# Performance work log

Hardware: AMD Instinct MI355X
Metric: run time of the kernel (lower is better)

Reference implementation:

```python
import jax, jax.numpy as jnp
import numpy as np

N_NODES = 50000
N_EDGES = 800000
IN_CH = 128
HEADS = 4
OUT_CH = 32
NEG_SLOPE = 0.2


def setup_inputs() -> dict:
    key = jax.random.key(0)
    ks = jax.random.split(key, 8)
    x = jax.random.normal(ks[0], (N_NODES, IN_CH), dtype=jnp.float32)
    # edges guaranteed to have no self-loops (module removes then re-adds them)
    tgt = jax.random.randint(ks[1], (N_EDGES,), 0, N_NODES)
    off = jax.random.randint(ks[2], (N_EDGES,), 1, N_NODES)
    src = (tgt + off) % N_NODES
    edge_index = jnp.stack([src, tgt]).astype(jnp.int64)
    glorot = lambda k, shp: jax.random.uniform(
        k, shp, jnp.float32, -1.0, 1.0) * np.sqrt(6.0 / (shp[-1] + shp[-2]))
    Wl = glorot(ks[3], (HEADS * OUT_CH, IN_CH))  # torch Linear weight [out,in]
    Wr = glorot(ks[4], (HEADS * OUT_CH, IN_CH))
    att = glorot(ks[5], (1, HEADS, OUT_CH))
    bl = jnp.zeros((HEADS * OUT_CH,), jnp.float32)
    br = jnp.zeros((HEADS * OUT_CH,), jnp.float32)
    bias = jnp.zeros((HEADS * OUT_CH,), jnp.float32)
    return {"x": x, "edge_index": edge_index, "Wl": Wl, "bl": bl,
            "Wr": Wr, "br": br, "att": att, "bias": bias}


def _forward(x, edge_index, Wl, bl, Wr, br, att, bias):
    H, C = HEADS, OUT_CH
    n = x.shape[0]
    x_l = (x @ Wl.T + bl).reshape(n, H, C)  # target projection
    x_r = (x @ Wr.T + br).reshape(n, H, C)  # source projection
    # add self-loops (inputs contain none by construction)
    loops = jnp.arange(n, dtype=edge_index.dtype)
    src = jnp.concatenate([edge_index[0], loops])
    tgt = jnp.concatenate([edge_index[1], loops])
    x_i = x_l[tgt]                     # [E', H, C]
    x_j = x_r[src]                     # [E', H, C]
    a_in = jax.nn.leaky_relu(x_i + x_j, NEG_SLOPE)
    alpha = jnp.einsum('ehc,ohc->eh', a_in, att)  # [E', H]
    # segment softmax over target nodes
    m = jax.ops.segment_max(alpha, tgt, num_segments=n)
    alpha = jnp.exp(alpha - jax.lax.stop_gradient(m)[tgt])
    denom = jax.ops.segment_sum(alpha, tgt, num_segments=n)
    alpha = alpha / denom[tgt]
    msgs = x_j * alpha[:, :, None]     # [E', H, C]
    out = jax.ops.segment_sum(msgs, tgt, num_segments=n)  # [N, H, C]
    out = out.reshape(n, H * C) + bias  # concat=True
    return out


def reference(x, edge_index, Wl, bl, Wr, br, att, bias):
    return _forward(x, edge_index, Wl, bl, Wr, br, att, bias)
```

## Files before the change

### kernel.cpp

```cpp
#include <hip/hip_runtime.h>
#include <hip/hip_bf16.h>
#include <stdint.h>

#define N_NODES 50000
#define N_EDGES 800000
#define IN_CH   128
#define NEG_SLOPE 0.2f

#define PROJ_BLOCKS 782
#define E_PER 8
#define FILL_BLOCKS 391

typedef short short8 __attribute__((ext_vector_type(8)));
typedef float f32x4  __attribute__((ext_vector_type(4)));
typedef float f32x2  __attribute__((ext_vector_type(2)));

static __device__ __forceinline__ float bf_lo(uint32_t p) { return __uint_as_float(p << 16); }
static __device__ __forceinline__ float bf_hi(uint32_t p) { return __uint_as_float(p & 0xffff0000u); }
static __device__ __forceinline__ uint16_t f_to_bf(float f) {
    uint32_t u = __float_as_uint(f);
    u += 0x7fffu + ((u >> 16) & 1u);
    return (uint16_t)(u >> 16);
}
static __device__ __forceinline__ float lrelu(float x) { return fmaxf(x, NEG_SLOPE * x); }

static __device__ __forceinline__ float sum16(float x) {
    x += __uint_as_float(__builtin_amdgcn_update_dpp(0, __float_as_uint(x), 0xB1,  0xf, 0xf, true));
    x += __uint_as_float(__builtin_amdgcn_update_dpp(0, __float_as_uint(x), 0x4E,  0xf, 0xf, true));
    x += __uint_as_float(__builtin_amdgcn_update_dpp(0, __float_as_uint(x), 0x141, 0xf, 0xf, true));
    x += __uint_as_float(__builtin_amdgcn_update_dpp(0, __float_as_uint(x), 0x140, 0xf, 0xf, true));
    return x;
}

__global__ __launch_bounds__(256) void prep_kernel(
    const float* __restrict__ Wl, const float* __restrict__ Wr,
    __hip_bfloat16* __restrict__ wswz, int* __restrict__ cnt)
{
    int t = blockIdx.x * 256 + threadIdx.x;
    if (t < 4096) {
        int ct = t >> 8, rem = t & 255;
        int ch = rem >> 6, lane = rem & 63;
        int m = lane & 15, quad = lane >> 4;
        const float* W = (ct < 8) ? Wl : Wr;
        int o = ((ct & 7) << 4) + m;
        const float* src = W + (size_t)o * IN_CH + ch * 32 + quad * 8;
        short8 f;
#pragma unroll
        for (int j = 0; j < 8; ++j) f[j] = (short)f_to_bf(src[j]);
        *(short8*)((short*)wswz + (size_t)t * 8) = f;
    }
    for (int i = t; i < N_NODES; i += 64 * 256) cnt[i] = 0;
}

__global__ __launch_bounds__(256) void mid_kernel(
    const float* __restrict__ x,
    const __hip_bfloat16* __restrict__ wswz,
    const float* __restrict__ bl, const float* __restrict__ br,
    float* __restrict__ xl, __hip_bfloat16* __restrict__ xr,
    const int* __restrict__ ei, int cap,
    int* __restrict__ cnt, uint16_t* __restrict__ csr)
{
    if (blockIdx.x < PROJ_BLOCKS) {
        int wave = blockIdx.x * 4 + (threadIdx.x >> 6);
        int rowbase = wave * 16;
        if (rowbase >= N_NODES) return;
        int lane = threadIdx.x & 63;
        int m = lane & 15;
        int quad = lane >> 4;

        short8 afrag[4];
        const float* xrow = x + (size_t)(rowbase + m) * IN_CH;
#pragma unroll
        for (int ch = 0; ch < 4; ++ch) {
            f32x4 p0 = *(const f32x4*)(xrow + ch * 32 + quad * 8);
            f32x4 p1 = *(const f32x4*)(xrow + ch * 32 + quad * 8 + 4);
            short8 f;
#pragma unroll
            for (int j = 0; j < 4; ++j) { f[j] = (short)f_to_bf(p0[j]); f[j + 4] = (short)f_to_bf(p1[j]); }
            afrag[ch] = f;
        }

        const short* wz = (const short*)wswz;
#pragma unroll
        for (int ct = 0; ct < 16; ++ct) {
            const float* bv = (ct < 8) ? bl : br;
            int o = ((ct & 7) << 4) + m;
            f32x4 acc = {0.f, 0.f, 0.f, 0.f};
#pragma unroll
            for (int ch = 0; ch < 4; ++ch) {
                short8 bfrag = *(const short8*)(wz + ((size_t)(ct * 4 + ch) * 64 + lane) * 8);
                acc = __builtin_amdgcn_mfma_f32_16x16x32_bf16(afrag[ch], bfrag, acc, 0, 0, 0);
            }
            float bias_v = bv[o];
            if (ct < 8) {
#pragma unroll
                for (int r = 0; r < 4; ++r)
                    xl[(size_t)(rowbase + quad * 4 + r) * IN_CH + o] = acc[r] + bias_v;
            } else {
#pragma unroll
                for (int r = 0; r < 4; ++r)
                    xr[(size_t)(rowbase + quad * 4 + r) * IN_CH + o] = __float2bfloat16(acc[r] + bias_v);
            }
        }
    } else {
        const uint32_t* eiw = (const uint32_t*)ei;
        bool z = (eiw[2 * (threadIdx.x & 63) + 1] == 0u);
        bool is64 = __popcll(__ballot(z)) >= 32;

        int tid = (blockIdx.x - PROJ_BLOCKS) * 256 + threadIdx.x;
        int e0 = tid * E_PER;
        if (e0 >= N_EDGES) return;

        int src[E_PER], tgt[E_PER];
        if (is64) {
            const int4* ps = (const int4*)(eiw + 2 * (size_t)e0);
            const int4* pt = (const int4*)(eiw + 2 * ((size_t)N_EDGES + e0));
#pragma unroll
            for (int k = 0; k < 4; ++k) {
                int4 s = ps[k], t = pt[k];
                src[2 * k] = s.x; src[2 * k + 1] = s.z;
                tgt[2 * k] = t.x; tgt[2 * k + 1] = t.z;
            }
        } else {
            const int4* ps = (const int4*)(ei + e0);
            const int4* pt = (const int4*)(ei + N_EDGES + e0);
#pragma unroll
            for (int k = 0; k < 2; ++k) {
                int4 s = ps[k], t = pt[k];
                src[4 * k] = s.x; src[4 * k + 1] = s.y; src[4 * k + 2] = s.z; src[4 * k + 3] = s.w;
                tgt[4 * k] = t.x; tgt[4 * k + 1] = t.y; tgt[4 * k + 2] = t.z; tgt[4 * k + 3] = t.w;
            }
        }

        int pos[E_PER];
#pragma unroll
        for (int k = 0; k < E_PER; ++k) {
            bool ok = (unsigned)src[k] < N_NODES && (unsigned)tgt[k] < N_NODES;
            pos[k] = ok ? atomicAdd(&cnt[tgt[k]], 1) : cap;
        }
#pragma unroll
        for (int k = 0; k < E_PER; ++k)
            if (pos[k] < cap)
                __builtin_nontemporal_store((uint16_t)src[k],
                                            &csr[(size_t)tgt[k] * cap + pos[k]]);
    }
}

__global__ __launch_bounds__(256) void agg_kernel(
    const __hip_bfloat16* __restrict__ xr,
    const int* __restrict__ cnt, const uint16_t* __restrict__ csr, int cap,
    const float* __restrict__ att, const float* __restrict__ bias,
    float* out )
{
    int n = blockIdx.x * 4 + (threadIdx.x >> 6);
    if (n >= N_NODES) return;
    int lane = threadIdx.x & 63;

    const uint32_t* xrw = (const uint32_t*)xr;

    f32x2 qv = *(const f32x2*)(out + (size_t)n * IN_CH + 2 * lane);
    f32x2 av = *(const f32x2*)(att + 2 * lane);
    f32x2 bv = *(const f32x2*)(bias + 2 * lane);

    int deg = min(cnt[n], cap);
    const uint16_t* lst = csr + (size_t)n * cap;
    int idxreg = (int)lst[min(lane, cap - 1)];

    uint32_t u = xrw[(size_t)n * 64 + lane];
    float v0 = bf_lo(u), v1 = bf_hi(u);
    float t = sum16(lrelu(qv[0] + v0) * av[0] + lrelu(qv[1] + v1) * av[1]);
    float w = __expf(t);
    float lsum = w;
    float acc0 = w * v0, acc1 = w * v1;

    if (deg > 0) {
        int dm1 = deg - 1;
        int s0a = __builtin_amdgcn_readlane(idxreg, 0);
        int s0b = __builtin_amdgcn_readlane(idxreg, min(1, dm1));
        int s1a = __builtin_amdgcn_readlane(idxreg, min(2, dm1));
        int s1b = __builtin_amdgcn_readlane(idxreg, min(3, dm1));
        uint32_t uA0 = xrw[(size_t)s0a * 64 + lane];
        uint32_t uB0 = xrw[(size_t)s0b * 64 + lane];
        uint32_t uA1 = xrw[(size_t)s1a * 64 + lane];
        uint32_t uB1 = xrw[(size_t)s1b * 64 + lane];
        int i = 0;
        while (i + 1 < deg) {
            int s2a = __builtin_amdgcn_readlane(idxreg, min(i + 4, dm1));
            int s2b = __builtin_amdgcn_readlane(idxreg, min(i + 5, dm1));
            uint32_t uA2 = xrw[(size_t)s2a * 64 + lane];
            uint32_t uB2 = xrw[(size_t)s2b * 64 + lane];

            float a0 = bf_lo(uA0), a1 = bf_hi(uA0);
            float b0 = bf_lo(uB0), b1 = bf_hi(uB0);
            float tA = sum16(lrelu(qv[0] + a0) * av[0] + lrelu(qv[1] + a1) * av[1]);
            float tB = sum16(lrelu(qv[0] + b0) * av[0] + lrelu(qv[1] + b1) * av[1]);
            float wA = __expf(tA), wB = __expf(tB);
            lsum += wA + wB;
            acc0 += wA * a0 + wB * b0;
            acc1 += wA * a1 + wB * b1;

            uA0 = uA1; uB0 = uB1;
            uA1 = uA2; uB1 = uB2;
            i += 2;
        }
        if (i < deg) {
            float a0 = bf_lo(uA0), a1 = bf_hi(uA0);
            float tA = sum16(lrelu(qv[0] + a0) * av[0] + lrelu(qv[1] + a1) * av[1]);
            float wA = __expf(tA);
            lsum += wA;
            acc0 += wA * a0;
            acc1 += wA * a1;
        }
    }

    float inv = 1.f / lsum;
    f32x2 ov;
    ov[0] = acc0 * inv + bv[0];
    ov[1] = acc1 * inv + bv[1];
    *(f32x2*)(out + (size_t)n * IN_CH + 2 * lane) = ov;
}

extern "C" void kernel_launch(void* const* d_in, const int* in_sizes, int n_in,
                              void* d_out, int out_size, void* d_ws, size_t ws_size,
                              hipStream_t stream) {
    const float* x    = (const float*)d_in[0];
    const int*   ei   = (const int*)d_in[1];
    const float* Wl   = (const float*)d_in[2];
    const float* bl   = (const float*)d_in[3];
    const float* Wr   = (const float*)d_in[4];
    const float* br   = (const float*)d_in[5];
    const float* att  = (const float*)d_in[6];
    const float* bias = (const float*)d_in[7];
    float* out = (float*)d_out;

    const size_t CSR_BASE = 13065536;
    char* ws = (char*)d_ws;
    __hip_bfloat16* xr   = (__hip_bfloat16*)(ws);
    __hip_bfloat16* wswz = (__hip_bfloat16*)(ws + 12800000);
    int*      cnt = (int*)(ws + 12865536);
    uint16_t* csr = (uint16_t*)(ws + CSR_BASE);

    long long avail = (ws_size > CSR_BASE) ? (long long)(ws_size - CSR_BASE) : 0;
    int cap = (int)(avail / ((long long)N_NODES * 2));
    if (cap > 64) cap = 64;
    if (cap < 1)  cap = 1;

    prep_kernel<<<64, 256, 0, stream>>>(Wl, Wr, wswz, cnt);
    mid_kernel<<<PROJ_BLOCKS + FILL_BLOCKS, 256, 0, stream>>>(
        x, wswz, bl, br, out, xr, ei, cap, cnt, csr);
    agg_kernel<<<N_NODES / 4, 256, 0, stream>>>(xr, cnt, csr, cap, att, bias, out);
}
```

Measured before the change: 195.6 us.

## Interleave per-node counter and neighbor list into one 128-byte slab

Packs each node's atomic degree counter and its bucketed source-index list into a single 128-byte slab, so the count and list share a cache line for both the atomic fill and the aggregation read. The list capacity drops from 64 to 62, and prep now zeroes the whole 6.4MB slab region instead of 200KB of counters. The nontemporal store is replaced by a normal store, which may keep lines cached near the atomics. The extra zeroing traffic and the lower capacity, which truncates nodes with more than 62 neighbours, are the trade-offs.

```diff
diff --git a/kernel.cpp b/kernel.cpp
--- a/kernel.cpp
+++ b/kernel.cpp
@@ -14,6 +14,7 @@
 typedef short short8 __attribute__((ext_vector_type(8)));
 typedef float f32x4  __attribute__((ext_vector_type(4)));
 typedef float f32x2  __attribute__((ext_vector_type(2)));
+typedef int   i32x4  __attribute__((ext_vector_type(4)));
 
 static __device__ __forceinline__ float bf_lo(uint32_t p) { return __uint_as_float(p << 16); }
 static __device__ __forceinline__ float bf_hi(uint32_t p) { return __uint_as_float(p & 0xffff0000u); }
@@ -34,7 +35,7 @@
 
 __global__ __launch_bounds__(256) void prep_kernel(
     const float* __restrict__ Wl, const float* __restrict__ Wr,
-    __hip_bfloat16* __restrict__ wswz, int* __restrict__ cnt)
+    __hip_bfloat16* __restrict__ wswz, i32x4* __restrict__ zbase, int zchunks)
 {
     int t = blockIdx.x * 256 + threadIdx.x;
     if (t < 4096) {
@@ -49,7 +50,8 @@
         for (int j = 0; j < 8; ++j) f[j] = (short)f_to_bf(src[j]);
         *(short8*)((short*)wswz + (size_t)t * 8) = f;
     }
-    for (int i = t; i < N_NODES; i += 64 * 256) cnt[i] = 0;
+    i32x4 z = {0, 0, 0, 0};
+    for (int i = t; i < zchunks; i += 64 * 256) zbase[i] = z;
 }
 
 __global__ __launch_bounds__(256) void mid_kernel(
@@ -58,7 +60,8 @@
     const float* __restrict__ bl, const float* __restrict__ br,
     float* __restrict__ xl, __hip_bfloat16* __restrict__ xr,
     const int* __restrict__ ei, int cap,
-    int* __restrict__ cnt, uint16_t* __restrict__ csr)
+    char* __restrict__ cbase, int cstride,
+    char* __restrict__ ebase, int estride)
 {
     if (blockIdx.x < PROJ_BLOCKS) {
         int wave = blockIdx.x * 4 + (threadIdx.x >> 6);
@@ -136,19 +139,20 @@
 #pragma unroll
         for (int k = 0; k < E_PER; ++k) {
             bool ok = (unsigned)src[k] < N_NODES && (unsigned)tgt[k] < N_NODES;
-            pos[k] = ok ? atomicAdd(&cnt[tgt[k]], 1) : cap;
+            pos[k] = ok ? atomicAdd((int*)(cbase + (size_t)tgt[k] * cstride), 1)
+                        : cap;
         }
 #pragma unroll
         for (int k = 0; k < E_PER; ++k)
             if (pos[k] < cap)
-                __builtin_nontemporal_store((uint16_t)src[k],
-                                            &csr[(size_t)tgt[k] * cap + pos[k]]);
+                *(uint16_t*)(ebase + (size_t)tgt[k] * estride + 2 * pos[k]) = (uint16_t)src[k];
     }
 }
 
 __global__ __launch_bounds__(256) void agg_kernel(
     const __hip_bfloat16* __restrict__ xr,
-    const int* __restrict__ cnt, const uint16_t* __restrict__ csr, int cap,
+    const char* __restrict__ cbase, int cstride,
+    const char* __restrict__ ebase, int estride, int cap,
     const float* __restrict__ att, const float* __restrict__ bias,
     float* out )
 {
@@ -162,8 +166,8 @@
     f32x2 av = *(const f32x2*)(att + 2 * lane);
     f32x2 bv = *(const f32x2*)(bias + 2 * lane);
 
-    int deg = min(cnt[n], cap);
-    const uint16_t* lst = csr + (size_t)n * cap;
+    int deg = min(*(const int*)(cbase + (size_t)n * cstride), cap);
+    const uint16_t* lst = (const uint16_t*)(ebase + (size_t)n * estride);
     int idxreg = (int)lst[min(lane, cap - 1)];
 
     uint32_t u = xrw[(size_t)n * 64 + lane];
@@ -233,20 +237,34 @@
     const float* bias = (const float*)d_in[7];
     float* out = (float*)d_out;
 
-    const size_t CSR_BASE = 13065536;
     char* ws = (char*)d_ws;
     __hip_bfloat16* xr   = (__hip_bfloat16*)(ws);
     __hip_bfloat16* wswz = (__hip_bfloat16*)(ws + 12800000);
-    int*      cnt = (int*)(ws + 12865536);
-    uint16_t* csr = (uint16_t*)(ws + CSR_BASE);
-
-    long long avail = (ws_size > CSR_BASE) ? (long long)(ws_size - CSR_BASE) : 0;
-    int cap = (int)(avail / ((long long)N_NODES * 2));
-    if (cap > 64) cap = 64;
-    if (cap < 1)  cap = 1;
-
-    prep_kernel<<<64, 256, 0, stream>>>(Wl, Wr, wswz, cnt);
+
+    const size_t SLAB_BASE = 12865536;
+    char* cbase; char* ebase;
+    int cstride, estride, cap;
+    size_t zbytes;
+    if (ws_size >= SLAB_BASE + (size_t)N_NODES * 128) {
+        cbase = ws + SLAB_BASE;  cstride = 128;
+        ebase = cbase + 4;       estride = 128;
+        cap = 62;
+        zbytes = (size_t)N_NODES * 128;
+    } else {
+        cbase = ws + SLAB_BASE;  cstride = 4;
+        ebase = ws + SLAB_BASE + 200000;
+        long long avail = (ws_size > SLAB_BASE + 200000)
+                        ? (long long)(ws_size - SLAB_BASE - 200000) : 0;
+        cap = (int)(avail / ((long long)N_NODES * 2));
+        if (cap > 64) cap = 64;
+        if (cap < 1)  cap = 1;
+        estride = 2 * cap;
+        zbytes = 200000;
+    }
+
+    prep_kernel<<<64, 256, 0, stream>>>(Wl, Wr, wswz, (i32x4*)cbase, (int)(zbytes / 16));
     mid_kernel<<<PROJ_BLOCKS + FILL_BLOCKS, 256, 0, stream>>>(
-        x, wswz, bl, br, out, xr, ei, cap, cnt, csr);
-    agg_kernel<<<N_NODES / 4, 256, 0, stream>>>(xr, cnt, csr, cap, att, bias, out);
-}
+        x, wswz, bl, br, out, xr, ei, cap, cbase, cstride, ebase, estride);
+    agg_kernel<<<N_NODES / 4, 256, 0, stream>>>(
+        xr, cbase, cstride, ebase, estride, cap, att, bias, out);
+}
```

New measurement: 180.9 us. -7.5%, faster.

## Build CSR via per-block LDS histograms, scan and scatter instead of global atomics

Applied to the files above, without the earlier changes.

Replaces the global-atomic counting fill with a three-pass counting sort. Each of B blocks builds a packed 8-bit per-node histogram of its edge slice in shared memory, a scan kernel turns the per-block histograms into offsets and packed degrees, and a scatter kernel writes source ids into a fixed 64-wide CSR using shared-memory atomics. The projection now runs as its own kernel. The aim is to avoid contended global atomics and their scattered writes. The cost is extra launches, low block counts in the histogram and scatter passes, loss of overlap between projection and fill, and degrees assumed to fit in 8 bits. The old path is kept as a fallback when the workspace is too small.

```diff
diff --git a/kernel.cpp b/kernel.cpp
--- a/kernel.cpp
+++ b/kernel.cpp
@@ -10,10 +10,12 @@
 #define PROJ_BLOCKS 782
 #define E_PER 8
 #define FILL_BLOCKS 391
+#define HIST_WORDS 12500
 
 typedef short short8 __attribute__((ext_vector_type(8)));
 typedef float f32x4  __attribute__((ext_vector_type(4)));
 typedef float f32x2  __attribute__((ext_vector_type(2)));
+typedef int   i32x4  __attribute__((ext_vector_type(4)));
 
 static __device__ __forceinline__ float bf_lo(uint32_t p) { return __uint_as_float(p << 16); }
 static __device__ __forceinline__ float bf_hi(uint32_t p) { return __uint_as_float(p & 0xffff0000u); }
@@ -32,76 +34,200 @@
     return x;
 }
 
-__global__ __launch_bounds__(256) void prep_kernel(
+static __device__ __forceinline__ void proj_body(
+    int wave, int lane,
+    const float* __restrict__ x, const __hip_bfloat16* __restrict__ wswz,
+    const float* __restrict__ bl, const float* __restrict__ br,
+    float* __restrict__ xl, __hip_bfloat16* __restrict__ xr)
+{
+    int rowbase = wave * 16;
+    if (rowbase >= N_NODES) return;
+    int m = lane & 15;
+    int quad = lane >> 4;
+
+    short8 afrag[4];
+    const float* xrow = x + (size_t)(rowbase + m) * IN_CH;
+#pragma unroll
+    for (int ch = 0; ch < 4; ++ch) {
+        f32x4 p0 = *(const f32x4*)(xrow + ch * 32 + quad * 8);
+        f32x4 p1 = *(const f32x4*)(xrow + ch * 32 + quad * 8 + 4);
+        short8 f;
+#pragma unroll
+        for (int j = 0; j < 4; ++j) { f[j] = (short)f_to_bf(p0[j]); f[j + 4] = (short)f_to_bf(p1[j]); }
+        afrag[ch] = f;
+    }
+
+    const short* wz = (const short*)wswz;
+#pragma unroll
+    for (int ct = 0; ct < 16; ++ct) {
+        const float* bv = (ct < 8) ? bl : br;
+        int o = ((ct & 7) << 4) + m;
+        f32x4 acc = {0.f, 0.f, 0.f, 0.f};
+#pragma unroll
+        for (int ch = 0; ch < 4; ++ch) {
+            short8 bfrag = *(const short8*)(wz + ((size_t)(ct * 4 + ch) * 64 + lane) * 8);
+            acc = __builtin_amdgcn_mfma_f32_16x16x32_bf16(afrag[ch], bfrag, acc, 0, 0, 0);
+        }
+        float bias_v = bv[o];
+        if (ct < 8) {
+#pragma unroll
+            for (int r = 0; r < 4; ++r)
+                xl[(size_t)(rowbase + quad * 4 + r) * IN_CH + o] = acc[r] + bias_v;
+        } else {
+#pragma unroll
+            for (int r = 0; r < 4; ++r)
+                xr[(size_t)(rowbase + quad * 4 + r) * IN_CH + o] = __float2bfloat16(acc[r] + bias_v);
+        }
+    }
+}
+
+static __device__ __forceinline__ void wswz_body(
+    int t, const float* __restrict__ Wl, const float* __restrict__ Wr,
+    __hip_bfloat16* __restrict__ wswz)
+{
+    int ct = t >> 8, rem = t & 255;
+    int ch = rem >> 6, lane = rem & 63;
+    int m = lane & 15, quad = lane >> 4;
+    const float* W = (ct < 8) ? Wl : Wr;
+    int o = ((ct & 7) << 4) + m;
+    const float* src = W + (size_t)o * IN_CH + ch * 32 + quad * 8;
+    short8 f;
+#pragma unroll
+    for (int j = 0; j < 8; ++j) f[j] = (short)f_to_bf(src[j]);
+    *(short8*)((short*)wswz + (size_t)t * 8) = f;
+}
+
+
+__global__ __launch_bounds__(256) void prep_sort(
+    const float* __restrict__ Wl, const float* __restrict__ Wr,
+    __hip_bfloat16* __restrict__ wswz,
+    const int* __restrict__ ei, uint32_t* __restrict__ H, int EPB)
+{
+    __shared__ uint32_t hist[HIST_WORDS];
+    int tid = threadIdx.x;
+    if (blockIdx.x < 16) {
+        wswz_body(blockIdx.x * 256 + tid, Wl, Wr, wswz);
+        return;
+    }
+    int fb = blockIdx.x - 16;
+    for (int w = tid; w < HIST_WORDS; w += 256) hist[w] = 0;
+    __syncthreads();
+
+    const uint32_t* eiw = (const uint32_t*)ei;
+    bool z = (eiw[2 * (tid & 63) + 1] == 0u);
+    bool is64 = __popcll(__ballot(z)) >= 32;
+    int e0 = fb * EPB;
+    if (is64) {
+        const uint2* e64 = (const uint2*)eiw;
+        for (int k = tid; k < EPB; k += 256) {
+            int e = e0 + k;
+            int s = (int)e64[e].x;
+            int t = (int)e64[(size_t)N_EDGES + e].x;
+            if ((unsigned)s < N_NODES && (unsigned)t < N_NODES)
+                atomicAdd(&hist[t >> 2], 1u << ((t & 3) * 8));
+        }
+    } else {
+        for (int k = tid; k < EPB; k += 256) {
+            int e = e0 + k;
+            int s = ei[e], t = ei[N_EDGES + e];
+            if ((unsigned)s < N_NODES && (unsigned)t < N_NODES)
+                atomicAdd(&hist[t >> 2], 1u << ((t & 3) * 8));
+        }
+    }
+    __syncthreads();
+    uint32_t* Hb = H + (size_t)fb * HIST_WORDS;
+    for (int w = tid; w < HIST_WORDS; w += 256) Hb[w] = hist[w];
+}
+
+__global__ __launch_bounds__(256) void proj_kernel(
+    const float* __restrict__ x, const __hip_bfloat16* __restrict__ wswz,
+    const float* __restrict__ bl, const float* __restrict__ br,
+    float* __restrict__ xl, __hip_bfloat16* __restrict__ xr)
+{
+    proj_body(blockIdx.x * 4 + (threadIdx.x >> 6), threadIdx.x & 63,
+              x, wswz, bl, br, xl, xr);
+}
+
+__global__ __launch_bounds__(256) void scan_kernel(
+    uint32_t* __restrict__ H, int B, uint32_t* __restrict__ degs)
+{
+    int w = blockIdx.x * 256 + threadIdx.x;
+    if (w >= HIST_WORDS) return;
+    uint32_t acc = 0;
+    for (int c = 0; c < B; c += 16) {
+        uint32_t v[16];
+#pragma unroll
+        for (int j = 0; j < 16; ++j) v[j] = H[(size_t)(c + j) * HIST_WORDS + w];
+#pragma unroll
+        for (int j = 0; j < 16; ++j) {
+            uint32_t t = v[j];
+            H[(size_t)(c + j) * HIST_WORDS + w] = acc;
+            acc += t;
+        }
+    }
+    degs[w] = acc;
+}
+
+__global__ __launch_bounds__(256) void scatter_kernel(
+    const int* __restrict__ ei, const uint32_t* __restrict__ H, int EPB,
+    uint16_t* __restrict__ csr)
+{
+    __shared__ uint32_t hist[HIST_WORDS];
+    int fb = blockIdx.x, tid = threadIdx.x;
+    const uint32_t* Hb = H + (size_t)fb * HIST_WORDS;
+    for (int w = tid; w < HIST_WORDS; w += 256) hist[w] = Hb[w];
+    __syncthreads();
+
+    const uint32_t* eiw = (const uint32_t*)ei;
+    bool z = (eiw[2 * (tid & 63) + 1] == 0u);
+    bool is64 = __popcll(__ballot(z)) >= 32;
+    int e0 = fb * EPB;
+    if (is64) {
+        const uint2* e64 = (const uint2*)eiw;
+        for (int k = tid; k < EPB; k += 256) {
+            int e = e0 + k;
+            int s = (int)e64[e].x;
+            int t = (int)e64[(size_t)N_EDGES + e].x;
+            if ((unsigned)s < N_NODES && (unsigned)t < N_NODES) {
+                uint32_t sh = (t & 3) * 8;
+                uint32_t old = atomicAdd(&hist[t >> 2], 1u << sh);
+                uint32_t pos = (old >> sh) & 255u;
+                if (pos < 64u) csr[(size_t)t * 64 + pos] = (uint16_t)s;
+            }
+        }
+    } else {
+        for (int k = tid; k < EPB; k += 256) {
+            int e = e0 + k;
+            int s = ei[e], t = ei[N_EDGES + e];
+            if ((unsigned)s < N_NODES && (unsigned)t < N_NODES) {
+                uint32_t sh = (t & 3) * 8;
+                uint32_t old = atomicAdd(&hist[t >> 2], 1u << sh);
+                uint32_t pos = (old >> sh) & 255u;
+                if (pos < 64u) csr[(size_t)t * 64 + pos] = (uint16_t)s;
+            }
+        }
+    }
+}
+
+__global__ __launch_bounds__(256) void prep_legacy(
     const float* __restrict__ Wl, const float* __restrict__ Wr,
     __hip_bfloat16* __restrict__ wswz, int* __restrict__ cnt)
 {
     int t = blockIdx.x * 256 + threadIdx.x;
-    if (t < 4096) {
-        int ct = t >> 8, rem = t & 255;
-        int ch = rem >> 6, lane = rem & 63;
-        int m = lane & 15, quad = lane >> 4;
-        const float* W = (ct < 8) ? Wl : Wr;
-        int o = ((ct & 7) << 4) + m;
-        const float* src = W + (size_t)o * IN_CH + ch * 32 + quad * 8;
-        short8 f;
-#pragma unroll
-        for (int j = 0; j < 8; ++j) f[j] = (short)f_to_bf(src[j]);
-        *(short8*)((short*)wswz + (size_t)t * 8) = f;
-    }
+    if (t < 4096) wswz_body(t, Wl, Wr, wswz);
     for (int i = t; i < N_NODES; i += 64 * 256) cnt[i] = 0;
 }
 
-__global__ __launch_bounds__(256) void mid_kernel(
-    const float* __restrict__ x,
-    const __hip_bfloat16* __restrict__ wswz,
+__global__ __launch_bounds__(256) void mid_legacy(
+    const float* __restrict__ x, const __hip_bfloat16* __restrict__ wswz,
     const float* __restrict__ bl, const float* __restrict__ br,
     float* __restrict__ xl, __hip_bfloat16* __restrict__ xr,
     const int* __restrict__ ei, int cap,
     int* __restrict__ cnt, uint16_t* __restrict__ csr)
 {
     if (blockIdx.x < PROJ_BLOCKS) {
-        int wave = blockIdx.x * 4 + (threadIdx.x >> 6);
-        int rowbase = wave * 16;
-        if (rowbase >= N_NODES) return;
-        int lane = threadIdx.x & 63;
-        int m = lane & 15;
-        int quad = lane >> 4;
-
-        short8 afrag[4];
-        const float* xrow = x + (size_t)(rowbase + m) * IN_CH;
-#pragma unroll
-        for (int ch = 0; ch < 4; ++ch) {
-            f32x4 p0 = *(const f32x4*)(xrow + ch * 32 + quad * 8);
-            f32x4 p1 = *(const f32x4*)(xrow + ch * 32 + quad * 8 + 4);
-            short8 f;
-#pragma unroll
-            for (int j = 0; j < 4; ++j) { f[j] = (short)f_to_bf(p0[j]); f[j + 4] = (short)f_to_bf(p1[j]); }
-            afrag[ch] = f;
-        }
-
-        const short* wz = (const short*)wswz;
-#pragma unroll
-        for (int ct = 0; ct < 16; ++ct) {
-            const float* bv = (ct < 8) ? bl : br;
-            int o = ((ct & 7) << 4) + m;
-            f32x4 acc = {0.f, 0.f, 0.f, 0.f};
-#pragma unroll
-            for (int ch = 0; ch < 4; ++ch) {
-                short8 bfrag = *(const short8*)(wz + ((size_t)(ct * 4 + ch) * 64 + lane) * 8);
-                acc = __builtin_amdgcn_mfma_f32_16x16x32_bf16(afrag[ch], bfrag, acc, 0, 0, 0);
-            }
-            float bias_v = bv[o];
-            if (ct < 8) {
-#pragma unroll
-                for (int r = 0; r < 4; ++r)
-                    xl[(size_t)(rowbase + quad * 4 + r) * IN_CH + o] = acc[r] + bias_v;
-            } else {
-#pragma unroll
-                for (int r = 0; r < 4; ++r)
-                    xr[(size_t)(rowbase + quad * 4 + r) * IN_CH + o] = __float2bfloat16(acc[r] + bias_v);
-            }
-        }
+        proj_body(blockIdx.x * 4 + (threadIdx.x >> 6), threadIdx.x & 63,
+                  x, wswz, bl, br, xl, xr);
     } else {
         const uint32_t* eiw = (const uint32_t*)ei;
         bool z = (eiw[2 * (threadIdx.x & 63) + 1] == 0u);
@@ -140,15 +266,14 @@
         }
 #pragma unroll
         for (int k = 0; k < E_PER; ++k)
-            if (pos[k] < cap)
-                __builtin_nontemporal_store((uint16_t)src[k],
-                                            &csr[(size_t)tgt[k] * cap + pos[k]]);
+            if (pos[k] < cap) csr[(size_t)tgt[k] * cap + pos[k]] = (uint16_t)src[k];
     }
 }
 
 __global__ __launch_bounds__(256) void agg_kernel(
     const __hip_bfloat16* __restrict__ xr,
-    const int* __restrict__ cnt, const uint16_t* __restrict__ csr, int cap,
+    const char* __restrict__ degbase, int degpacked,
+    const uint16_t* __restrict__ csr, int ldcsr, int cap,
     const float* __restrict__ att, const float* __restrict__ bias,
     float* out )
 {
@@ -162,8 +287,16 @@
     f32x2 av = *(const f32x2*)(att + 2 * lane);
     f32x2 bv = *(const f32x2*)(bias + 2 * lane);
 
-    int deg = min(cnt[n], cap);
-    const uint16_t* lst = csr + (size_t)n * cap;
+    int deg;
+    if (degpacked) {
+        uint32_t pk = ((const uint32_t*)degbase)[n >> 2];
+        deg = (int)((pk >> ((n & 3) * 8)) & 255u);
+    } else {
+        deg = *(const int*)(degbase + (size_t)n * 4);
+    }
+    deg = min(deg, cap);
+
+    const uint16_t* lst = csr + (size_t)n * ldcsr;
     int idxreg = (int)lst[min(lane, cap - 1)];
 
     uint32_t u = xrw[(size_t)n * 64 + lane];
@@ -233,20 +366,44 @@
     const float* bias = (const float*)d_in[7];
     float* out = (float*)d_out;
 
-    const size_t CSR_BASE = 13065536;
     char* ws = (char*)d_ws;
     __hip_bfloat16* xr   = (__hip_bfloat16*)(ws);
     __hip_bfloat16* wswz = (__hip_bfloat16*)(ws + 12800000);
-    int*      cnt = (int*)(ws + 12865536);
-    uint16_t* csr = (uint16_t*)(ws + CSR_BASE);
-
-    long long avail = (ws_size > CSR_BASE) ? (long long)(ws_size - CSR_BASE) : 0;
-    int cap = (int)(avail / ((long long)N_NODES * 2));
-    if (cap > 64) cap = 64;
-    if (cap < 1)  cap = 1;
-
-    prep_kernel<<<64, 256, 0, stream>>>(Wl, Wr, wswz, cnt);
-    mid_kernel<<<PROJ_BLOCKS + FILL_BLOCKS, 256, 0, stream>>>(
-        x, wswz, bl, br, out, xr, ei, cap, cnt, csr);
-    agg_kernel<<<N_NODES / 4, 256, 0, stream>>>(xr, cnt, csr, cap, att, bias, out);
-}
+    const size_t AFTER = 12865536;
+
+    int B = 0;
+    {
+        size_t need64 = AFTER + (size_t)64 * 50000 + 50048 + 6400000;
+        size_t need16 = AFTER + (size_t)16 * 50000 + 50048 + 6400000;
+        if (ws_size >= need64) B = 64;
+        else if (ws_size >= need16) B = 16;
+    }
+
+    if (B) {
+        uint32_t* H    = (uint32_t*)(ws + AFTER);
+        uint32_t* degs = (uint32_t*)(ws + AFTER + (size_t)B * 50000);
+        uint16_t* csr  = (uint16_t*)(ws + AFTER + (size_t)B * 50000 + 50048);
+        int EPB = N_EDGES / B;
+
+        prep_sort<<<16 + B, 256, 0, stream>>>(Wl, Wr, wswz, ei, H, EPB);
+        proj_kernel<<<PROJ_BLOCKS, 256, 0, stream>>>(x, wswz, bl, br, out, xr);
+        scan_kernel<<<49, 256, 0, stream>>>(H, B, degs);
+        scatter_kernel<<<B, 256, 0, stream>>>(ei, H, EPB, csr);
+        agg_kernel<<<N_NODES / 4, 256, 0, stream>>>(
+            xr, (const char*)degs, 1, csr, 64, 64, att, bias, out);
+    } else {
+        int* cnt      = (int*)(ws + AFTER);
+        uint16_t* csr = (uint16_t*)(ws + AFTER + 200000);
+        long long avail = (ws_size > AFTER + 200000)
+                        ? (long long)(ws_size - AFTER - 200000) : 0;
+        int cap = (int)(avail / ((long long)N_NODES * 2));
+        if (cap > 64) cap = 64;
+        if (cap < 1)  cap = 1;
+
+        prep_legacy<<<64, 256, 0, stream>>>(Wl, Wr, wswz, cnt);
+        mid_legacy<<<PROJ_BLOCKS + FILL_BLOCKS, 256, 0, stream>>>(
+            x, wswz, bl, br, out, xr, ei, cap, cnt, csr);
+        agg_kernel<<<N_NODES / 4, 256, 0, stream>>>(
+            xr, (const char*)cnt, 0, csr, cap, cap, att, bias, out);
+    }
+}
```

Measured after the change: 203.3 us. 3.9% more time.

## Split fused projection/CSR kernel and vectorize aggregation with packed math and paired DPP reductions

Applied to the files above, without the earlier changes.

Splits the merged projection-plus-CSR-fill kernel into separate fill and projection launches. The projection now gives each block 16 rows with the four waves sharing the column tiles, rather than each wave computing all 16 tiles. The aggregation loop switches to f32x2 packed arithmetic and an inline-asm DPP reduction that interleaves two edge scores, aiming to hide DPP latency. The CSR store loses its nontemporal hint, the split adds a launch and removes the overlap between fill and projection, and each wave now redoes the x-fragment load and bf16 conversion.

```diff
diff --git a/kernel.cpp b/kernel.cpp
--- a/kernel.cpp
+++ b/kernel.cpp
@@ -7,7 +7,6 @@
 #define IN_CH   128
 #define NEG_SLOPE 0.2f
 
-#define PROJ_BLOCKS 782
 #define E_PER 8
 #define FILL_BLOCKS 391
 
@@ -22,7 +21,14 @@
     u += 0x7fffu + ((u >> 16) & 1u);
     return (uint16_t)(u >> 16);
 }
-static __device__ __forceinline__ float lrelu(float x) { return fmaxf(x, NEG_SLOPE * x); }
+
+static __device__ __forceinline__ f32x2 lrelu2(f32x2 x) {
+    f32x2 s = x * NEG_SLOPE;
+    f32x2 r;
+    r[0] = fmaxf(x[0], s[0]);
+    r[1] = fmaxf(x[1], s[1]);
+    return r;
+}
 
 static __device__ __forceinline__ float sum16(float x) {
     x += __uint_as_float(__builtin_amdgcn_update_dpp(0, __float_as_uint(x), 0xB1,  0xf, 0xf, true));
@@ -30,6 +36,19 @@
     x += __uint_as_float(__builtin_amdgcn_update_dpp(0, __float_as_uint(x), 0x141, 0xf, 0xf, true));
     x += __uint_as_float(__builtin_amdgcn_update_dpp(0, __float_as_uint(x), 0x140, 0xf, 0xf, true));
     return x;
+}
+
+static __device__ __forceinline__ void sum16x2(float& a, float& b) {
+    asm("s_nop 0\n\t"
+        "v_add_f32 %0, %0, %0 quad_perm:[1,0,3,2] row_mask:0xf bank_mask:0xf bound_ctrl:0\n\t"
+        "v_add_f32 %1, %1, %1 quad_perm:[1,0,3,2] row_mask:0xf bank_mask:0xf bound_ctrl:0\n\t"
+        "v_add_f32 %0, %0, %0 quad_perm:[2,3,0,1] row_mask:0xf bank_mask:0xf bound_ctrl:0\n\t"
+        "v_add_f32 %1, %1, %1 quad_perm:[2,3,0,1] row_mask:0xf bank_mask:0xf bound_ctrl:0\n\t"
+        "v_add_f32 %0, %0, %0 row_half_mirror row_mask:0xf bank_mask:0xf bound_ctrl:0\n\t"
+        "v_add_f32 %1, %1, %1 row_half_mirror row_mask:0xf bank_mask:0xf bound_ctrl:0\n\t"
+        "v_add_f32 %0, %0, %0 row_mirror row_mask:0xf bank_mask:0xf bound_ctrl:0\n\t"
+        "v_add_f32 %1, %1, %1 row_mirror row_mask:0xf bank_mask:0xf bound_ctrl:0"
+        : "+v"(a), "+v"(b));
 }
 
 __global__ __launch_bounds__(256) void prep_kernel(
@@ -52,97 +71,95 @@
     for (int i = t; i < N_NODES; i += 64 * 256) cnt[i] = 0;
 }
 
-__global__ __launch_bounds__(256) void mid_kernel(
-    const float* __restrict__ x,
-    const __hip_bfloat16* __restrict__ wswz,
-    const float* __restrict__ bl, const float* __restrict__ br,
-    float* __restrict__ xl, __hip_bfloat16* __restrict__ xr,
+__global__ __launch_bounds__(256) void fill_kernel(
     const int* __restrict__ ei, int cap,
     int* __restrict__ cnt, uint16_t* __restrict__ csr)
 {
-    if (blockIdx.x < PROJ_BLOCKS) {
-        int wave = blockIdx.x * 4 + (threadIdx.x >> 6);
-        int rowbase = wave * 16;
-        if (rowbase >= N_NODES) return;
-        int lane = threadIdx.x & 63;
-        int m = lane & 15;
-        int quad = lane >> 4;
-
-        short8 afrag[4];
-        const float* xrow = x + (size_t)(rowbase + m) * IN_CH;
+    const uint32_t* eiw = (const uint32_t*)ei;
+    bool z = (eiw[2 * (threadIdx.x & 63) + 1] == 0u);
+    bool is64 = __popcll(__ballot(z)) >= 32;
+
+    int tid = blockIdx.x * 256 + threadIdx.x;
+    int e0 = tid * E_PER;
+    if (e0 >= N_EDGES) return;
+
+    int src[E_PER], tgt[E_PER];
+    if (is64) {
+        const int4* ps = (const int4*)(eiw + 2 * (size_t)e0);
+        const int4* pt = (const int4*)(eiw + 2 * ((size_t)N_EDGES + e0));
+#pragma unroll
+        for (int k = 0; k < 4; ++k) {
+            int4 s = ps[k], t = pt[k];
+            src[2 * k] = s.x; src[2 * k + 1] = s.z;
+            tgt[2 * k] = t.x; tgt[2 * k + 1] = t.z;
+        }
+    } else {
+        const int4* ps = (const int4*)(ei + e0);
+        const int4* pt = (const int4*)(ei + N_EDGES + e0);
+#pragma unroll
+        for (int k = 0; k < 2; ++k) {
+            int4 s = ps[k], t = pt[k];
+            src[4 * k] = s.x; src[4 * k + 1] = s.y; src[4 * k + 2] = s.z; src[4 * k + 3] = s.w;
+            tgt[4 * k] = t.x; tgt[4 * k + 1] = t.y; tgt[4 * k + 2] = t.z; tgt[4 * k + 3] = t.w;
+        }
+    }
+
+    int pos[E_PER];
+#pragma unroll
+    for (int k = 0; k < E_PER; ++k) {
+        bool ok = (unsigned)src[k] < N_NODES && (unsigned)tgt[k] < N_NODES;
+        pos[k] = ok ? atomicAdd(&cnt[tgt[k]], 1) : cap;
+    }
+#pragma unroll
+    for (int k = 0; k < E_PER; ++k)
+        if (pos[k] < cap) csr[(size_t)tgt[k] * cap + pos[k]] = (uint16_t)src[k];
+}
+
+__global__ __launch_bounds__(256) void proj_kernel(
+    const float* __restrict__ x, const __hip_bfloat16* __restrict__ wswz,
+    const float* __restrict__ bl, const float* __restrict__ br,
+    float* __restrict__ xl, __hip_bfloat16* __restrict__ xr)
+{
+    int rowbase = blockIdx.x * 16;
+    int lane = threadIdx.x & 63;
+    int widx = threadIdx.x >> 6;
+    int m = lane & 15;
+    int quad = lane >> 4;
+
+    short8 afrag[4];
+    const float* xrow = x + (size_t)(rowbase + m) * IN_CH;
+#pragma unroll
+    for (int ch = 0; ch < 4; ++ch) {
+        f32x4 p0 = *(const f32x4*)(xrow + ch * 32 + quad * 8);
+        f32x4 p1 = *(const f32x4*)(xrow + ch * 32 + quad * 8 + 4);
+        short8 f;
+#pragma unroll
+        for (int j = 0; j < 4; ++j) { f[j] = (short)f_to_bf(p0[j]); f[j + 4] = (short)f_to_bf(p1[j]); }
+        afrag[ch] = f;
+    }
+
+    const short* wz = (const short*)wswz;
+    const float* bv = (widx < 2) ? bl : br;
+#pragma unroll
+    for (int cc = 0; cc < 4; ++cc) {
+        int ct = widx * 4 + cc;
+        int o = ((ct & 7) << 4) + m;
+        f32x4 acc = {0.f, 0.f, 0.f, 0.f};
 #pragma unroll
         for (int ch = 0; ch < 4; ++ch) {
-            f32x4 p0 = *(const f32x4*)(xrow + ch * 32 + quad * 8);
-            f32x4 p1 = *(const f32x4*)(xrow + ch * 32 + quad * 8 + 4);
-            short8 f;
-#pragma unroll
-            for (int j = 0; j < 4; ++j) { f[j] = (short)f_to_bf(p0[j]); f[j + 4] = (short)f_to_bf(p1[j]); }
-            afrag[ch] = f;
-        }
-
-        const short* wz = (const short*)wswz;
-#pragma unroll
-        for (int ct = 0; ct < 16; ++ct) {
-            const float* bv = (ct < 8) ? bl : br;
-            int o = ((ct & 7) << 4) + m;
-            f32x4 acc = {0.f, 0.f, 0.f, 0.f};
-#pragma unroll
-            for (int ch = 0; ch < 4; ++ch) {
-                short8 bfrag = *(const short8*)(wz + ((size_t)(ct * 4 + ch) * 64 + lane) * 8);
-                acc = __builtin_amdgcn_mfma_f32_16x16x32_bf16(afrag[ch], bfrag, acc, 0, 0, 0);
-            }
-            float bias_v = bv[o];
-            if (ct < 8) {
-#pragma unroll
-                for (int r = 0; r < 4; ++r)
-                    xl[(size_t)(rowbase + quad * 4 + r) * IN_CH + o] = acc[r] + bias_v;
-            } else {
-#pragma unroll
-                for (int r = 0; r < 4; ++r)
-                    xr[(size_t)(rowbase + quad * 4 + r) * IN_CH + o] = __float2bfloat16(acc[r] + bias_v);
-            }
-        }
-    } else {
-        const uint32_t* eiw = (const uint32_t*)ei;
-        bool z = (eiw[2 * (threadIdx.x & 63) + 1] == 0u);
-        bool is64 = __popcll(__ballot(z)) >= 32;
-
-        int tid = (blockIdx.x - PROJ_BLOCKS) * 256 + threadIdx.x;
-        int e0 = tid * E_PER;
-        if (e0 >= N_EDGES) return;
-
-        int src[E_PER], tgt[E_PER];
-        if (is64) {
-            const int4* ps = (const int4*)(eiw + 2 * (size_t)e0);
-            const int4* pt = (const int4*)(eiw + 2 * ((size_t)N_EDGES + e0));
-#pragma unroll
-            for (int k = 0; k < 4; ++k) {
-                int4 s = ps[k], t = pt[k];
-                src[2 * k] = s.x; src[2 * k + 1] = s.z;
-                tgt[2 * k] = t.x; tgt[2 * k + 1] = t.z;
-            }
+            short8 bfrag = *(const short8*)(wz + ((size_t)(ct * 4 + ch) * 64 + lane) * 8);
+            acc = __builtin_amdgcn_mfma_f32_16x16x32_bf16(afrag[ch], bfrag, acc, 0, 0, 0);
+        }
+        float bias_v = bv[o];
+        if (widx < 2) {
+#pragma unroll
+            for (int r = 0; r < 4; ++r)
+                xl[(size_t)(rowbase + quad * 4 + r) * IN_CH + o] = acc[r] + bias_v;
         } else {
-            const int4* ps = (const int4*)(ei + e0);
-            const int4* pt = (const int4*)(ei + N_EDGES + e0);
-#pragma unroll
-            for (int k = 0; k < 2; ++k) {
-                int4 s = ps[k], t = pt[k];
-                src[4 * k] = s.x; src[4 * k + 1] = s.y; src[4 * k + 2] = s.z; src[4 * k + 3] = s.w;
-                tgt[4 * k] = t.x; tgt[4 * k + 1] = t.y; tgt[4 * k + 2] = t.z; tgt[4 * k + 3] = t.w;
-            }
-        }
-
-        int pos[E_PER];
-#pragma unroll
-        for (int k = 0; k < E_PER; ++k) {
-            bool ok = (unsigned)src[k] < N_NODES && (unsigned)tgt[k] < N_NODES;
-            pos[k] = ok ? atomicAdd(&cnt[tgt[k]], 1) : cap;
-        }
-#pragma unroll
-        for (int k = 0; k < E_PER; ++k)
-            if (pos[k] < cap)
-                __builtin_nontemporal_store((uint16_t)src[k],
-                                            &csr[(size_t)tgt[k] * cap + pos[k]]);
+#pragma unroll
+            for (int r = 0; r < 4; ++r)
+                xr[(size_t)(rowbase + quad * 4 + r) * IN_CH + o] = __float2bfloat16(acc[r] + bias_v);
+        }
     }
 }
 
@@ -167,11 +184,12 @@
     int idxreg = (int)lst[min(lane, cap - 1)];
 
     uint32_t u = xrw[(size_t)n * 64 + lane];
-    float v0 = bf_lo(u), v1 = bf_hi(u);
-    float t = sum16(lrelu(qv[0] + v0) * av[0] + lrelu(qv[1] + v1) * av[1]);
+    f32x2 a0v; a0v[0] = bf_lo(u); a0v[1] = bf_hi(u);
+    f32x2 p0 = lrelu2(qv + a0v) * av;
+    float t = sum16(p0[0] + p0[1]);
     float w = __expf(t);
     float lsum = w;
-    float acc0 = w * v0, acc1 = w * v1;
+    f32x2 acc = w * a0v;
 
     if (deg > 0) {
         int dm1 = deg - 1;
@@ -190,33 +208,34 @@
             uint32_t uA2 = xrw[(size_t)s2a * 64 + lane];
             uint32_t uB2 = xrw[(size_t)s2b * 64 + lane];
 
-            float a0 = bf_lo(uA0), a1 = bf_hi(uA0);
-            float b0 = bf_lo(uB0), b1 = bf_hi(uB0);
-            float tA = sum16(lrelu(qv[0] + a0) * av[0] + lrelu(qv[1] + a1) * av[1]);
-            float tB = sum16(lrelu(qv[0] + b0) * av[0] + lrelu(qv[1] + b1) * av[1]);
+            f32x2 aA; aA[0] = bf_lo(uA0); aA[1] = bf_hi(uA0);
+            f32x2 aB; aB[0] = bf_lo(uB0); aB[1] = bf_hi(uB0);
+            f32x2 pA = lrelu2(qv + aA) * av;
+            f32x2 pB = lrelu2(qv + aB) * av;
+            float tA = pA[0] + pA[1];
+            float tB = pB[0] + pB[1];
+            sum16x2(tA, tB);
             float wA = __expf(tA), wB = __expf(tB);
             lsum += wA + wB;
-            acc0 += wA * a0 + wB * b0;
-            acc1 += wA * a1 + wB * b1;
+            acc += wA * aA;
+            acc += wB * aB;
 
             uA0 = uA1; uB0 = uB1;
             uA1 = uA2; uB1 = uB2;
             i += 2;
         }
         if (i < deg) {
-            float a0 = bf_lo(uA0), a1 = bf_hi(uA0);
-            float tA = sum16(lrelu(qv[0] + a0) * av[0] + lrelu(qv[1] + a1) * av[1]);
+            f32x2 aA; aA[0] = bf_lo(uA0); aA[1] = bf_hi(uA0);
+            f32x2 pA = lrelu2(qv + aA) * av;
+            float tA = sum16(pA[0] + pA[1]);
             float wA = __expf(tA);
             lsum += wA;
-            acc0 += wA * a0;
-            acc1 += wA * a1;
+            acc += wA * aA;
         }
     }
 
     float inv = 1.f / lsum;
-    f32x2 ov;
-    ov[0] = acc0 * inv + bv[0];
-    ov[1] = acc1 * inv + bv[1];
+    f32x2 ov = acc * inv + bv;
     *(f32x2*)(out + (size_t)n * IN_CH + 2 * lane) = ov;
 }
 
@@ -246,7 +265,7 @@
     if (cap < 1)  cap = 1;
 
     prep_kernel<<<64, 256, 0, stream>>>(Wl, Wr, wswz, cnt);
-    mid_kernel<<<PROJ_BLOCKS + FILL_BLOCKS, 256, 0, stream>>>(
-        x, wswz, bl, br, out, xr, ei, cap, cnt, csr);
+    fill_kernel<<<FILL_BLOCKS, 256, 0, stream>>>(ei, cap, cnt, csr);
+    proj_kernel<<<N_NODES / 16, 256, 0, stream>>>(x, wswz, bl, br, out, xr);
     agg_kernel<<<N_NODES / 4, 256, 0, stream>>>(xr, cnt, csr, cap, att, bias, out);
 }
```

Result: faster. 190.9 us (-2.4%).
